# Performance work log

Measured on AMD Instinct MI355X. Metric: run time of the kernel, lower is better.

The kernel has to match this reference:

```python
import jax, jax.numpy as jnp
import numpy as np
import math

D = 512          # belief_dim
H = 128          # hidden_dim
R = 64           # relation_dim
M = 8192         # max_beliefs
N = 131072       # candidate pairs
INIT_BIAS = math.log(0.4 / 0.6) * -1.0  # = log(1.5) ~ 0.405465


def _linear_params(key, fan_in, fan_out):
    kw, kb = jax.random.split(key)
    bound = 1.0 / math.sqrt(fan_in)
    W = jax.random.uniform(kw, (fan_in, fan_out), minval=-bound, maxval=bound, dtype=jnp.float32)
    b = jax.random.uniform(kb, (fan_out,), minval=-bound, maxval=bound, dtype=jnp.float32)
    return W, b


def setup_inputs() -> dict:
    key = jax.random.key(0)
    ks = jax.random.split(key, 11)
    beliefs = jax.random.normal(ks[0], (M, D), dtype=jnp.float32)
    src_idx = jax.random.randint(ks[1], (N,), 0, M)
    tgt_idx = jax.random.randint(ks[2], (N,), 0, M)
    # proposal_net: 3D -> H -> H//2 -> 1  (last bias = log(1.5))
    pw1, pb1 = _linear_params(ks[3], 3 * D, H)
    pw2, pb2 = _linear_params(ks[4], H, H // 2)
    pw3, _ = _linear_params(ks[5], H // 2, 1)
    pb3 = jnp.full((1,), INIT_BIAS, dtype=jnp.float32)
    # direction_net: 3D -> H//2 -> 1 (sigmoid)
    dw1, db1 = _linear_params(ks[6], 3 * D, H // 2)
    dw2, db2 = _linear_params(ks[7], H // 2, 1)
    # relation_net: 3D -> H -> R
    rw1, rb1 = _linear_params(ks[8], 3 * D, H)
    rw2, rb2 = _linear_params(ks[9], H, R)
    return {
        "beliefs": beliefs, "src_idx": src_idx, "tgt_idx": tgt_idx,
        "pw1": pw1, "pb1": pb1, "pw2": pw2, "pb2": pb2, "pw3": pw3, "pb3": pb3,
        "dw1": dw1, "db1": db1, "dw2": dw2, "db2": db2,
        "rw1": rw1, "rb1": rb1, "rw2": rw2, "rb2": rb2,
    }


def reference(beliefs, src_idx, tgt_idx,
              pw1, pb1, pw2, pb2, pw3, pb3,
              dw1, db1, dw2, db2,
              rw1, rb1, rw2, rb2):
    src = beliefs[src_idx]                       # [N, D] gather
    tgt = beliefs[tgt_idx]                       # [N, D] gather
    feats = jnp.concatenate([src, tgt, jnp.abs(src - tgt)], axis=-1)  # [N, 3D]

    # proposal head -> edge probability
    h = jax.nn.relu(feats @ pw1 + pb1)
    h = jax.nn.relu(h @ pw2 + pb2)
    probs = jax.nn.sigmoid((h @ pw3 + pb3)[:, 0])                     # [N]

    # direction head -> angle in [0, pi/2]
    d = jax.nn.relu(feats @ dw1 + db1)
    directions = jax.nn.sigmoid((d @ dw2 + db2)[:, 0]) * (jnp.pi / 2)  # [N]

    # relation head -> initial relation vectors
    r = jax.nn.relu(feats @ rw1 + rb1)
    relations = r @ rw2 + rb2                                          # [N, R]

    return probs, directions, relations
```

## Files before the change

kernel.cpp:

```cpp
#include <hip/hip_runtime.h>
#include <hip/hip_bf16.h>


#define DD 512
#define K3 1536
#define ROWS 128
#define LDACT 328
#define LDH 72
#define BUFS 12288

typedef short bf16x8 __attribute__((ext_vector_type(8)));
typedef float f32x4 __attribute__((ext_vector_type(4)));

__device__ inline float b2f(short s) {
    union { float f; unsigned u; } v;
    v.u = ((unsigned)(unsigned short)s) << 16;
    return v.f;
}
__device__ inline short f2b(float f) {
    union { float fl; unsigned u; } v;
    v.fl = f;
    unsigned x = v.u;
    unsigned r = x + 0x7fffu + ((x >> 16) & 1u);
    return (short)(r >> 16);
}
__device__ inline short babsdiff(short a, short b) {
    union { float f; unsigned u; } v;
    v.f = b2f(a) - b2f(b);
    return (short)((v.u & 0x7fffffffu) >> 16);
}

__device__ __forceinline__ int sidx32(int seg, int rt, int lane) {
    return ((seg * 8 + rt) * 64 + lane) * 8;
}

__device__ __forceinline__ void writeStage(short* buf, int rtw, int lnw, int kcb,
                                           bf16x8 s0, bf16x8 s1,
                                           bf16x8 t0, bf16x8 t1) {
    bf16x8 a0, a1;
#pragma unroll
    for (int j = 0; j < 8; j++) {
        a0[j] = babsdiff(s0[j], t0[j]);
        a1[j] = babsdiff(s1[j], t1[j]);
    }
    int l0 = kcb * 16 + lnw, l1 = l0 + 16;
    *(bf16x8*)&buf[sidx32(0, rtw, l0)] = s0;
    *(bf16x8*)&buf[sidx32(0, rtw, l1)] = s1;
    *(bf16x8*)&buf[sidx32(1, rtw, l0)] = t0;
    *(bf16x8*)&buf[sidx32(1, rtw, l1)] = t1;
    *(bf16x8*)&buf[sidx32(2, rtw, l0)] = a0;
    *(bf16x8*)&buf[sidx32(2, rtw, l1)] = a1;
}

__device__ __forceinline__ void stage_f32(const float* bs, const float* bt,
                                          short* buf, int rtw, int lnw, int kcb) {
#pragma unroll
    for (int c = 0; c < 2; c++) {
        bf16x8 sb, tb, ab;
#pragma unroll
        for (int h = 0; h < 2; h++) {
            float4 s4 = ((const float4*)bs)[c * 2 + h];
            float4 t4 = ((const float4*)bt)[c * 2 + h];
            float ss[4] = {s4.x, s4.y, s4.z, s4.w};
            float tt[4] = {t4.x, t4.y, t4.z, t4.w};
#pragma unroll
            for (int e = 0; e < 4; e++) {
                int j = h * 4 + e;
                sb[j] = f2b(ss[e]);
                tb[j] = f2b(tt[e]);
                ab[j] = f2b(fabsf(ss[e] - tt[e]));
            }
        }
        int l16 = (kcb + c) * 16 + lnw;
        *(bf16x8*)&buf[sidx32(0, rtw, l16)] = sb;
        *(bf16x8*)&buf[sidx32(1, rtw, l16)] = tb;
        *(bf16x8*)&buf[sidx32(2, rtw, l16)] = ab;
    }
}

#define WT_ELEMS (320 * 1536)
#define P2T_OFF WT_ELEMS
#define R2T_OFF (WT_ELEMS + 64 * 128)
#define PREP_TOT (WT_ELEMS + 2 * 64 * 128)
#define BEL_ELEMS (8192 * 512)
#define BEL_OFF PREP_TOT

__global__ void prep_kernel(const float* __restrict__ pw1,
                            const float* __restrict__ dw1,
                            const float* __restrict__ rw1,
                            const float* __restrict__ pw2,
                            const float* __restrict__ rw2,
                            const float* __restrict__ beliefs,
                            short* __restrict__ ws, int total8) {
    int i8 = blockIdx.x * 256 + threadIdx.x;
    if (i8 >= total8) return;
    int i = i8 * 8;
    bf16x8 o;
    if (i < WT_ELEMS) {
        int n = i / K3, k = i - n * K3;
        const float* src;
        int stride, off;
        if (n < 128)      { src = pw1; stride = 128; off = n; }
        else if (n < 192) { src = dw1; stride = 64;  off = n - 128; }
        else              { src = rw1; stride = 128; off = n - 192; }
#pragma unroll
        for (int j = 0; j < 8; j++) o[j] = f2b(src[(k + j) * stride + off]);
    } else if (i < R2T_OFF) {
        int jj = i - P2T_OFF;
        int n = jj >> 7, k = jj & 127;
#pragma unroll
        for (int j = 0; j < 8; j++) o[j] = f2b(pw2[(k + j) * 64 + n]);
    } else if (i < PREP_TOT) {
        int jj = i - R2T_OFF;
        int n = jj >> 7, k = jj & 127;
#pragma unroll
        for (int j = 0; j < 8; j++) o[j] = f2b(rw2[(k + j) * 64 + n]);
    } else {
        const float4* b4 = (const float4*)(beliefs + (i - BEL_OFF));
        float4 x = b4[0], y = b4[1];
        float v[8] = {x.x, x.y, x.z, x.w, y.x, y.y, y.z, y.w};
#pragma unroll
        for (int j = 0; j < 8; j++) o[j] = f2b(v[j]);
    }
    *(bf16x8*)&ws[i] = o;
}

template<bool BF>
__global__ __launch_bounds__(256, 2) void edge_main(
    const float* __restrict__ beliefs, const short* __restrict__ bel16,
    const int* __restrict__ src_idx, const int* __restrict__ tgt_idx,
    const float* __restrict__ pb1, const float* __restrict__ db1,
    const float* __restrict__ rb1,
    const float* __restrict__ pb2, const float* __restrict__ pw3,
    const float* __restrict__ pb3,
    const float* __restrict__ dw2, const float* __restrict__ db2,
    const float* __restrict__ rb2,
    const short* __restrict__ WT, const short* __restrict__ pw2T,
    const short* __restrict__ rw2T,
    float* __restrict__ out, int N)
{
    __shared__ __align__(16) char smem_u[49152];
    __shared__ __align__(16) short h2s[64][LDH];
    __shared__ int sIdx[ROWS], tIdx[ROWS];

    short* As2 = (short*)smem_u;
    short (*acts)[LDACT] = (short (*)[LDACT])smem_u;

    const int t = threadIdx.x;
    const int r0 = blockIdx.x * ROWS;
    const int w = t >> 6, lane = t & 63, q = lane >> 4, ln = lane & 15;

    if (t < ROWS) sIdx[t] = src_idx[r0 + t] * DD;
    else tIdx[t - ROWS] = tgt_idx[r0 + t - ROWS] * DD;
    __syncthreads();

    f32x4 acc[5][8];
#pragma unroll
    for (int ct = 0; ct < 5; ct++)
#pragma unroll
        for (int rt = 0; rt < 8; rt++) acc[ct][rt] = (f32x4)(0.f);

    const int rrow = t >> 1, kh = t & 1;
    const int rtw = rrow >> 4, lnw = rrow & 15;
    const int kcb = kh * 2;
    const int srow = sIdx[rrow], trow = tIdx[rrow];

    if constexpr (BF) {
        const bf16x8* pS = (const bf16x8*)(bel16 + srow + kh * 16);
        const bf16x8* pT = (const bf16x8*)(bel16 + trow + kh * 16);
        writeStage(As2, rtw, lnw, kcb, pS[0], pS[1], pT[0], pT[1]);
    } else {
        stage_f32(beliefs + srow + kh * 16, beliefs + trow + kh * 16,
                  As2, rtw, lnw, kcb);
    }
    __syncthreads();

    for (int step = 0; step < 16; ++step) {
        short* bufC = As2 + (step & 1) * BUFS;
        short* bufN = As2 + ((step & 1) ^ 1) * BUFS;
        const int k0 = step * 32;
        const bool pf = (step < 15);
        bf16x8 ns0, ns1, nt0, nt1;

#pragma unroll
        for (int seg = 0; seg < 3; seg++) {
            bf16x8 bfr[5];
#pragma unroll
            for (int ct = 0; ct < 5; ct++) {
                int col = w * 80 + ct * 16 + ln;
                bfr[ct] = *(const bf16x8*)(WT + (size_t)col * K3 +
                                           seg * DD + k0 + q * 8);
            }
            if (seg == 2) {
                __builtin_amdgcn_sched_barrier(0);
                if constexpr (BF) {
                    if (pf) {
                        const bf16x8* pS = (const bf16x8*)(bel16 + srow + k0 + 32 + kh * 16);
                        const bf16x8* pT = (const bf16x8*)(bel16 + trow + k0 + 32 + kh * 16);
                        ns0 = pS[0]; ns1 = pS[1]; nt0 = pT[0]; nt1 = pT[1];
                    }
                }
                __builtin_amdgcn_sched_barrier(0);
            }
#pragma unroll
            for (int rt = 0; rt < 8; rt++) {
                bf16x8 af = *(const bf16x8*)&bufC[sidx32(seg, rt, lane)];
#pragma unroll
                for (int ct = 0; ct < 5; ct++)
                    acc[ct][rt] = __builtin_amdgcn_mfma_f32_16x16x32_bf16(
                        af, bfr[ct], acc[ct][rt], 0, 0, 0);
            }
        }
        if constexpr (BF) {
            if (pf) writeStage(bufN, rtw, lnw, kcb, ns0, ns1, nt0, nt1);
        } else {
            if (pf) stage_f32(beliefs + srow + k0 + 32 + kh * 16,
                              beliefs + trow + k0 + 32 + kh * 16,
                              bufN, rtw, lnw, kcb);
        }
        __syncthreads();
    }

#pragma unroll
    for (int h = 0; h < 2; h++) {
#pragma unroll
        for (int ct = 0; ct < 5; ct++) {
            int col = w * 80 + ct * 16 + ln;
            float bias = (col < 128) ? pb1[col]
                       : (col < 192) ? db1[col - 128]
                                     : rb1[col - 192];
#pragma unroll
            for (int rt4 = 0; rt4 < 4; rt4++)
#pragma unroll
                for (int i = 0; i < 4; i++) {
                    int lrow = rt4 * 16 + q * 4 + i;
                    float v = acc[ct][h * 4 + rt4][i] + bias;
                    acts[lrow][col] = f2b(fmaxf(v, 0.f));
                }
        }
        __syncthreads();

        {
            f32x4 rc[4];
#pragma unroll
            for (int rt = 0; rt < 4; rt++) rc[rt] = (f32x4)(0.f);
#pragma unroll
            for (int ks = 0; ks < 4; ks++) {
                bf16x8 bfr = *(const bf16x8*)(rw2T + (w * 16 + ln) * 128 +
                                              ks * 32 + q * 8);
#pragma unroll
                for (int rt = 0; rt < 4; rt++) {
                    bf16x8 afr = *(const bf16x8*)&acts[rt * 16 + ln][192 + ks * 32 + q * 8];
                    rc[rt] = __builtin_amdgcn_mfma_f32_16x16x32_bf16(afr, bfr, rc[rt], 0, 0, 0);
                }
            }
            int col = w * 16 + ln;
            float bias = rb2[col];
            float* rel = out + 2 * (size_t)N;
#pragma unroll
            for (int rt = 0; rt < 4; rt++)
#pragma unroll
                for (int i = 0; i < 4; i++) {
                    int grow = r0 + h * 64 + rt * 16 + q * 4 + i;
                    rel[(size_t)grow * 64 + col] = rc[rt][i] + bias;
                }
        }

        {
            f32x4 pc[4];
#pragma unroll
            for (int rt = 0; rt < 4; rt++) pc[rt] = (f32x4)(0.f);
#pragma unroll
            for (int ks = 0; ks < 4; ks++) {
                bf16x8 bfr = *(const bf16x8*)(pw2T + (w * 16 + ln) * 128 +
                                              ks * 32 + q * 8);
#pragma unroll
                for (int rt = 0; rt < 4; rt++) {
                    bf16x8 afr = *(const bf16x8*)&acts[rt * 16 + ln][0 + ks * 32 + q * 8];
                    pc[rt] = __builtin_amdgcn_mfma_f32_16x16x32_bf16(afr, bfr, pc[rt], 0, 0, 0);
                }
            }
            int col = w * 16 + ln;
            float bias = pb2[col];
#pragma unroll
            for (int rt = 0; rt < 4; rt++)
#pragma unroll
                for (int i = 0; i < 4; i++) {
                    int lrow = rt * 16 + q * 4 + i;
                    h2s[lrow][col] = f2b(fmaxf(pc[rt][i] + bias, 0.f));
                }
        }
        __syncthreads();

        if (t < 64) {
            float s = pb3[0];
#pragma unroll 8
            for (int k = 0; k < 64; k++) s += b2f(h2s[t][k]) * pw3[k];
            float pr = 1.f / (1.f + __expf(-s));
            out[r0 + h * 64 + t] = pr;
        } else if (t < 128) {
            int lrow = t - 64;
            float s = db2[0];
#pragma unroll 8
            for (int k = 0; k < 64; k++) s += b2f(acts[lrow][128 + k]) * dw2[k];
            float dir = (1.f / (1.f + __expf(-s))) * 1.57079632679489662f;
            out[(size_t)N + r0 + h * 64 + lrow] = dir;
        }
        __syncthreads();
    }
}

extern "C" void kernel_launch(void* const* d_in, const int* in_sizes, int n_in,
                              void* d_out, int out_size, void* d_ws, size_t ws_size,
                              hipStream_t stream) {
    const float* beliefs = (const float*)d_in[0];
    const int* src = (const int*)d_in[1];
    const int* tgt = (const int*)d_in[2];
    const float* pw1 = (const float*)d_in[3];
    const float* pb1 = (const float*)d_in[4];
    const float* pw2 = (const float*)d_in[5];
    const float* pb2 = (const float*)d_in[6];
    const float* pw3 = (const float*)d_in[7];
    const float* pb3 = (const float*)d_in[8];
    const float* dw1 = (const float*)d_in[9];
    const float* db1 = (const float*)d_in[10];
    const float* dw2 = (const float*)d_in[11];
    const float* db2 = (const float*)d_in[12];
    const float* rw1 = (const float*)d_in[13];
    const float* rb1 = (const float*)d_in[14];
    const float* rw2 = (const float*)d_in[15];
    const float* rb2 = (const float*)d_in[16];

    short* ws = (short*)d_ws;
    short* WT    = ws;
    short* pw2T  = ws + P2T_OFF;
    short* rw2T  = ws + R2T_OFF;
    short* bel16 = ws + BEL_OFF;
    const int N = in_sizes[1];

    const bool useBf = ws_size >= (size_t)(PREP_TOT + BEL_ELEMS) * sizeof(short);
    const int prepElems = useBf ? (PREP_TOT + BEL_ELEMS) : PREP_TOT;
    const int prep8 = prepElems / 8;

    prep_kernel<<<(prep8 + 255) / 256, 256, 0, stream>>>(
        pw1, dw1, rw1, pw2, rw2, beliefs, ws, prep8);

    if (useBf)
        edge_main<true><<<N / ROWS, 256, 0, stream>>>(
            beliefs, bel16, src, tgt, pb1, db1, rb1, pb2, pw3, pb3,
            dw2, db2, rb2, WT, pw2T, rw2T, (float*)d_out, N);
    else
        edge_main<false><<<N / ROWS, 256, 0, stream>>>(
            beliefs, bel16, src, tgt, pb1, db1, rb1, pb2, pw3, pb3,
            dw2, db2, rb2, WT, pw2T, rw2T, (float*)d_out, N);
}
```

Baseline: 270.3 us.

## Fold auxiliary LDS into main buffer for 3 blocks/CU, prefetch weights, set MFMA priority

Removes the separate h2s and index LDS arrays by aliasing them into the main shared buffer. This brings LDS per block down to 48KB so launch bounds can request 3 blocks per CU. An extra barrier is added to keep the aliasing safe. The seg-0 weight fragments for the next k-step are prefetched a step ahead, and the MFMA loop is wrapped in s_setprio. The risk is register pressure: the 160-float accumulator and the extra prefetch registers must fit under the tighter occupancy target, or the code may spill.

```diff
diff --git a/kernel.cpp b/kernel.cpp
--- a/kernel.cpp
+++ b/kernel.cpp
@@ -6,7 +6,6 @@
 #define K3 1536
 #define ROWS 128
 #define LDACT 328
-#define LDH 72
 #define BUFS 12288
 
 typedef short bf16x8 __attribute__((ext_vector_type(8)));
@@ -126,7 +125,7 @@
 }
 
 template<bool BF>
-__global__ __launch_bounds__(256, 2) void edge_main(
+__global__ __launch_bounds__(256, 3) void edge_main(
     const float* __restrict__ beliefs, const short* __restrict__ bel16,
     const int* __restrict__ src_idx, const int* __restrict__ tgt_idx,
     const float* __restrict__ pb1, const float* __restrict__ db1,
@@ -140,11 +139,11 @@
     float* __restrict__ out, int N)
 {
     __shared__ __align__(16) char smem_u[49152];
-    __shared__ __align__(16) short h2s[64][LDH];
-    __shared__ int sIdx[ROWS], tIdx[ROWS];
 
     short* As2 = (short*)smem_u;
     short (*acts)[LDACT] = (short (*)[LDACT])smem_u;
+    int* sIdx = (int*)smem_u;
+    int* tIdx = sIdx + ROWS;
 
     const int t = threadIdx.x;
     const int r0 = blockIdx.x * ROWS;
@@ -153,18 +152,25 @@
     if (t < ROWS) sIdx[t] = src_idx[r0 + t] * DD;
     else tIdx[t - ROWS] = tgt_idx[r0 + t - ROWS] * DD;
     __syncthreads();
-
-    f32x4 acc[5][8];
-#pragma unroll
-    for (int ct = 0; ct < 5; ct++)
-#pragma unroll
-        for (int rt = 0; rt < 8; rt++) acc[ct][rt] = (f32x4)(0.f);
 
     const int rrow = t >> 1, kh = t & 1;
     const int rtw = rrow >> 4, lnw = rrow & 15;
     const int kcb = kh * 2;
     const int srow = sIdx[rrow], trow = tIdx[rrow];
-
+    __syncthreads();
+
+    f32x4 acc[5][8];
+#pragma unroll
+    for (int ct = 0; ct < 5; ct++)
+#pragma unroll
+        for (int rt = 0; rt < 8; rt++) acc[ct][rt] = (f32x4)(0.f);
+
+    bf16x8 bfr0[5];
+#pragma unroll
+    for (int ct = 0; ct < 5; ct++) {
+        int col = w * 80 + ct * 16 + ln;
+        bfr0[ct] = *(const bf16x8*)(WT + (size_t)col * K3 + q * 8);
+    }
     if constexpr (BF) {
         const bf16x8* pS = (const bf16x8*)(bel16 + srow + kh * 16);
         const bf16x8* pT = (const bf16x8*)(bel16 + trow + kh * 16);
@@ -185,23 +191,35 @@
 #pragma unroll
         for (int seg = 0; seg < 3; seg++) {
             bf16x8 bfr[5];
-#pragma unroll
-            for (int ct = 0; ct < 5; ct++) {
-                int col = w * 80 + ct * 16 + ln;
-                bfr[ct] = *(const bf16x8*)(WT + (size_t)col * K3 +
-                                           seg * DD + k0 + q * 8);
+            if (seg == 0) {
+#pragma unroll
+                for (int ct = 0; ct < 5; ct++) bfr[ct] = bfr0[ct];
+            } else {
+#pragma unroll
+                for (int ct = 0; ct < 5; ct++) {
+                    int col = w * 80 + ct * 16 + ln;
+                    bfr[ct] = *(const bf16x8*)(WT + (size_t)col * K3 +
+                                               seg * DD + k0 + q * 8);
+                }
             }
             if (seg == 2) {
                 __builtin_amdgcn_sched_barrier(0);
-                if constexpr (BF) {
-                    if (pf) {
+                if (pf) {
+                    if constexpr (BF) {
                         const bf16x8* pS = (const bf16x8*)(bel16 + srow + k0 + 32 + kh * 16);
                         const bf16x8* pT = (const bf16x8*)(bel16 + trow + k0 + 32 + kh * 16);
                         ns0 = pS[0]; ns1 = pS[1]; nt0 = pT[0]; nt1 = pT[1];
                     }
+#pragma unroll
+                    for (int ct = 0; ct < 5; ct++) {
+                        int col = w * 80 + ct * 16 + ln;
+                        bfr0[ct] = *(const bf16x8*)(WT + (size_t)col * K3 +
+                                                    k0 + 32 + q * 8);
+                    }
                 }
                 __builtin_amdgcn_sched_barrier(0);
             }
+            __builtin_amdgcn_s_setprio(1);
 #pragma unroll
             for (int rt = 0; rt < 8; rt++) {
                 bf16x8 af = *(const bf16x8*)&bufC[sidx32(seg, rt, lane)];
@@ -210,6 +228,7 @@
                     acc[ct][rt] = __builtin_amdgcn_mfma_f32_16x16x32_bf16(
                         af, bfr[ct], acc[ct][rt], 0, 0, 0);
             }
+            __builtin_amdgcn_s_setprio(0);
         }
         if constexpr (BF) {
             if (pf) writeStage(bufN, rtw, lnw, kcb, ns0, ns1, nt0, nt1);
@@ -266,8 +285,8 @@
                 }
         }
 
+        f32x4 pc[4];
         {
-            f32x4 pc[4];
 #pragma unroll
             for (int rt = 0; rt < 4; rt++) pc[rt] = (f32x4)(0.f);
 #pragma unroll
@@ -280,6 +299,10 @@
                     pc[rt] = __builtin_amdgcn_mfma_f32_16x16x32_bf16(afr, bfr, pc[rt], 0, 0, 0);
                 }
             }
+        }
+        __syncthreads();
+
+        {
             int col = w * 16 + ln;
             float bias = pb2[col];
 #pragma unroll
@@ -287,7 +310,7 @@
 #pragma unroll
                 for (int i = 0; i < 4; i++) {
                     int lrow = rt * 16 + q * 4 + i;
-                    h2s[lrow][col] = f2b(fmaxf(pc[rt][i] + bias, 0.f));
+                    acts[lrow][col] = f2b(fmaxf(pc[rt][i] + bias, 0.f));
                 }
         }
         __syncthreads();
@@ -295,7 +318,7 @@
         if (t < 64) {
             float s = pb3[0];
 #pragma unroll 8
-            for (int k = 0; k < 64; k++) s += b2f(h2s[t][k]) * pw3[k];
+            for (int k = 0; k < 64; k++) s += b2f(acts[t][k]) * pw3[k];
             float pr = 1.f / (1.f + __expf(-s));
             out[r0 + h * 64 + t] = pr;
         } else if (t < 128) {
```

Result: slower. 963.5 us (+256.5%).

## Halve rows per block to 64 and raise occupancy to three blocks per CU

Applied to the files above, without the earlier changes.

Each block now handles 64 candidate rows instead of 128. This halves the accumulator registers and the staging buffers, and the h2s and index arrays are folded into the shared activation buffer so LDS use drops to about 41KB. The launch bounds are raised to 3 blocks per CU to hide gather latency, and s_setprio is added around the MFMA loops. The cost is that each block reuses the weight tiles loaded from global/L2 over half as many rows, doubling total weight traffic.

```diff
diff --git a/kernel.cpp b/kernel.cpp
--- a/kernel.cpp
+++ b/kernel.cpp
@@ -4,10 +4,9 @@
 
 #define DD 512
 #define K3 1536
-#define ROWS 128
+#define RB 64
 #define LDACT 328
-#define LDH 72
-#define BUFS 12288
+#define BUFS 6144
 
 typedef short bf16x8 __attribute__((ext_vector_type(8)));
 typedef float f32x4 __attribute__((ext_vector_type(4)));
@@ -30,52 +29,36 @@
     return (short)((v.u & 0x7fffffffu) >> 16);
 }
 
-__device__ __forceinline__ int sidx32(int seg, int rt, int lane) {
-    return ((seg * 8 + rt) * 64 + lane) * 8;
-}
-
-__device__ __forceinline__ void writeStage(short* buf, int rtw, int lnw, int kcb,
-                                           bf16x8 s0, bf16x8 s1,
-                                           bf16x8 t0, bf16x8 t1) {
-    bf16x8 a0, a1;
-#pragma unroll
-    for (int j = 0; j < 8; j++) {
-        a0[j] = babsdiff(s0[j], t0[j]);
-        a1[j] = babsdiff(s1[j], t1[j]);
-    }
-    int l0 = kcb * 16 + lnw, l1 = l0 + 16;
-    *(bf16x8*)&buf[sidx32(0, rtw, l0)] = s0;
-    *(bf16x8*)&buf[sidx32(0, rtw, l1)] = s1;
-    *(bf16x8*)&buf[sidx32(1, rtw, l0)] = t0;
-    *(bf16x8*)&buf[sidx32(1, rtw, l1)] = t1;
-    *(bf16x8*)&buf[sidx32(2, rtw, l0)] = a0;
-    *(bf16x8*)&buf[sidx32(2, rtw, l1)] = a1;
+__device__ __forceinline__ int sidx4(int seg, int rt, int lane) {
+    return ((seg * 4 + rt) * 64 + lane) * 8;
+}
+
+__device__ __forceinline__ void writeStage(short* buf, int rtw, int lpos,
+                                           bf16x8 s8, bf16x8 t8) {
+    bf16x8 a8;
+#pragma unroll
+    for (int j = 0; j < 8; j++) a8[j] = babsdiff(s8[j], t8[j]);
+    *(bf16x8*)&buf[sidx4(0, rtw, lpos)] = s8;
+    *(bf16x8*)&buf[sidx4(1, rtw, lpos)] = t8;
+    *(bf16x8*)&buf[sidx4(2, rtw, lpos)] = a8;
 }
 
 __device__ __forceinline__ void stage_f32(const float* bs, const float* bt,
-                                          short* buf, int rtw, int lnw, int kcb) {
-#pragma unroll
-    for (int c = 0; c < 2; c++) {
-        bf16x8 sb, tb, ab;
-#pragma unroll
-        for (int h = 0; h < 2; h++) {
-            float4 s4 = ((const float4*)bs)[c * 2 + h];
-            float4 t4 = ((const float4*)bt)[c * 2 + h];
-            float ss[4] = {s4.x, s4.y, s4.z, s4.w};
-            float tt[4] = {t4.x, t4.y, t4.z, t4.w};
-#pragma unroll
-            for (int e = 0; e < 4; e++) {
-                int j = h * 4 + e;
-                sb[j] = f2b(ss[e]);
-                tb[j] = f2b(tt[e]);
-                ab[j] = f2b(fabsf(ss[e] - tt[e]));
-            }
-        }
-        int l16 = (kcb + c) * 16 + lnw;
-        *(bf16x8*)&buf[sidx32(0, rtw, l16)] = sb;
-        *(bf16x8*)&buf[sidx32(1, rtw, l16)] = tb;
-        *(bf16x8*)&buf[sidx32(2, rtw, l16)] = ab;
-    }
+                                          short* buf, int rtw, int lpos) {
+    bf16x8 s8, t8;
+#pragma unroll
+    for (int h = 0; h < 2; h++) {
+        float4 s4 = ((const float4*)bs)[h];
+        float4 t4 = ((const float4*)bt)[h];
+        float ss[4] = {s4.x, s4.y, s4.z, s4.w};
+        float tt[4] = {t4.x, t4.y, t4.z, t4.w};
+#pragma unroll
+        for (int e = 0; e < 4; e++) {
+            s8[h * 4 + e] = f2b(ss[e]);
+            t8[h * 4 + e] = f2b(tt[e]);
+        }
+    }
+    writeStage(buf, rtw, lpos, s8, t8);
 }
 
 #define WT_ELEMS (320 * 1536)
@@ -126,7 +109,7 @@
 }
 
 template<bool BF>
-__global__ __launch_bounds__(256, 2) void edge_main(
+__global__ __launch_bounds__(256, 3) void edge_main(
     const float* __restrict__ beliefs, const short* __restrict__ bel16,
     const int* __restrict__ src_idx, const int* __restrict__ tgt_idx,
     const float* __restrict__ pb1, const float* __restrict__ db1,
@@ -139,39 +122,40 @@
     const short* __restrict__ rw2T,
     float* __restrict__ out, int N)
 {
-    __shared__ __align__(16) char smem_u[49152];
-    __shared__ __align__(16) short h2s[64][LDH];
-    __shared__ int sIdx[ROWS], tIdx[ROWS];
+    __shared__ __align__(16) char smem_u[41984];
 
     short* As2 = (short*)smem_u;
     short (*acts)[LDACT] = (short (*)[LDACT])smem_u;
+    int* sIdx = (int*)smem_u;
+    int* tIdx = sIdx + RB;
 
     const int t = threadIdx.x;
-    const int r0 = blockIdx.x * ROWS;
+    const int r0 = blockIdx.x * RB;
     const int w = t >> 6, lane = t & 63, q = lane >> 4, ln = lane & 15;
 
-    if (t < ROWS) sIdx[t] = src_idx[r0 + t] * DD;
-    else tIdx[t - ROWS] = tgt_idx[r0 + t - ROWS] * DD;
-    __syncthreads();
-
-    f32x4 acc[5][8];
+    if (t < RB) sIdx[t] = src_idx[r0 + t] * DD;
+    else if (t < 2 * RB) tIdx[t - RB] = tgt_idx[r0 + t - RB] * DD;
+    __syncthreads();
+
+    const int rr = t >> 2, cc = t & 3;
+    const int rtw = rr >> 4;
+    const int lpos = cc * 16 + (rr & 15);
+    const int srow = sIdx[rr], trow = tIdx[rr];
+    __syncthreads();
+
+    f32x4 acc[5][4];
 #pragma unroll
     for (int ct = 0; ct < 5; ct++)
 #pragma unroll
-        for (int rt = 0; rt < 8; rt++) acc[ct][rt] = (f32x4)(0.f);
-
-    const int rrow = t >> 1, kh = t & 1;
-    const int rtw = rrow >> 4, lnw = rrow & 15;
-    const int kcb = kh * 2;
-    const int srow = sIdx[rrow], trow = tIdx[rrow];
+        for (int rt = 0; rt < 4; rt++) acc[ct][rt] = (f32x4)(0.f);
 
     if constexpr (BF) {
-        const bf16x8* pS = (const bf16x8*)(bel16 + srow + kh * 16);
-        const bf16x8* pT = (const bf16x8*)(bel16 + trow + kh * 16);
-        writeStage(As2, rtw, lnw, kcb, pS[0], pS[1], pT[0], pT[1]);
+        bf16x8 s8 = *(const bf16x8*)(bel16 + srow + cc * 8);
+        bf16x8 t8 = *(const bf16x8*)(bel16 + trow + cc * 8);
+        writeStage(As2, rtw, lpos, s8, t8);
     } else {
-        stage_f32(beliefs + srow + kh * 16, beliefs + trow + kh * 16,
-                  As2, rtw, lnw, kcb);
+        stage_f32(beliefs + srow + cc * 8, beliefs + trow + cc * 8,
+                  As2, rtw, lpos);
     }
     __syncthreads();
 
@@ -180,7 +164,7 @@
         short* bufN = As2 + ((step & 1) ^ 1) * BUFS;
         const int k0 = step * 32;
         const bool pf = (step < 15);
-        bf16x8 ns0, ns1, nt0, nt1;
+        bf16x8 ns8, nt8;
 
 #pragma unroll
         for (int seg = 0; seg < 3; seg++) {
@@ -193,120 +177,121 @@
             }
             if (seg == 2) {
                 __builtin_amdgcn_sched_barrier(0);
-                if constexpr (BF) {
-                    if (pf) {
-                        const bf16x8* pS = (const bf16x8*)(bel16 + srow + k0 + 32 + kh * 16);
-                        const bf16x8* pT = (const bf16x8*)(bel16 + trow + k0 + 32 + kh * 16);
-                        ns0 = pS[0]; ns1 = pS[1]; nt0 = pT[0]; nt1 = pT[1];
+                if (pf) {
+                    if constexpr (BF) {
+                        ns8 = *(const bf16x8*)(bel16 + srow + k0 + 32 + cc * 8);
+                        nt8 = *(const bf16x8*)(bel16 + trow + k0 + 32 + cc * 8);
                     }
                 }
                 __builtin_amdgcn_sched_barrier(0);
             }
-#pragma unroll
-            for (int rt = 0; rt < 8; rt++) {
-                bf16x8 af = *(const bf16x8*)&bufC[sidx32(seg, rt, lane)];
+            __builtin_amdgcn_s_setprio(1);
+#pragma unroll
+            for (int rt = 0; rt < 4; rt++) {
+                bf16x8 af = *(const bf16x8*)&bufC[sidx4(seg, rt, lane)];
 #pragma unroll
                 for (int ct = 0; ct < 5; ct++)
                     acc[ct][rt] = __builtin_amdgcn_mfma_f32_16x16x32_bf16(
                         af, bfr[ct], acc[ct][rt], 0, 0, 0);
             }
+            __builtin_amdgcn_s_setprio(0);
         }
         if constexpr (BF) {
-            if (pf) writeStage(bufN, rtw, lnw, kcb, ns0, ns1, nt0, nt1);
+            if (pf) writeStage(bufN, rtw, lpos, ns8, nt8);
         } else {
-            if (pf) stage_f32(beliefs + srow + k0 + 32 + kh * 16,
-                              beliefs + trow + k0 + 32 + kh * 16,
-                              bufN, rtw, lnw, kcb);
+            if (pf) stage_f32(beliefs + srow + k0 + 32 + cc * 8,
+                              beliefs + trow + k0 + 32 + cc * 8,
+                              bufN, rtw, lpos);
         }
         __syncthreads();
     }
 
 #pragma unroll
-    for (int h = 0; h < 2; h++) {
-#pragma unroll
-        for (int ct = 0; ct < 5; ct++) {
-            int col = w * 80 + ct * 16 + ln;
-            float bias = (col < 128) ? pb1[col]
-                       : (col < 192) ? db1[col - 128]
-                                     : rb1[col - 192];
-#pragma unroll
-            for (int rt4 = 0; rt4 < 4; rt4++)
-#pragma unroll
-                for (int i = 0; i < 4; i++) {
-                    int lrow = rt4 * 16 + q * 4 + i;
-                    float v = acc[ct][h * 4 + rt4][i] + bias;
-                    acts[lrow][col] = f2b(fmaxf(v, 0.f));
-                }
-        }
-        __syncthreads();
-
-        {
-            f32x4 rc[4];
-#pragma unroll
-            for (int rt = 0; rt < 4; rt++) rc[rt] = (f32x4)(0.f);
-#pragma unroll
-            for (int ks = 0; ks < 4; ks++) {
-                bf16x8 bfr = *(const bf16x8*)(rw2T + (w * 16 + ln) * 128 +
-                                              ks * 32 + q * 8);
-#pragma unroll
-                for (int rt = 0; rt < 4; rt++) {
-                    bf16x8 afr = *(const bf16x8*)&acts[rt * 16 + ln][192 + ks * 32 + q * 8];
-                    rc[rt] = __builtin_amdgcn_mfma_f32_16x16x32_bf16(afr, bfr, rc[rt], 0, 0, 0);
-                }
-            }
-            int col = w * 16 + ln;
-            float bias = rb2[col];
-            float* rel = out + 2 * (size_t)N;
-#pragma unroll
-            for (int rt = 0; rt < 4; rt++)
-#pragma unroll
-                for (int i = 0; i < 4; i++) {
-                    int grow = r0 + h * 64 + rt * 16 + q * 4 + i;
-                    rel[(size_t)grow * 64 + col] = rc[rt][i] + bias;
-                }
-        }
-
-        {
-            f32x4 pc[4];
-#pragma unroll
-            for (int rt = 0; rt < 4; rt++) pc[rt] = (f32x4)(0.f);
-#pragma unroll
-            for (int ks = 0; ks < 4; ks++) {
-                bf16x8 bfr = *(const bf16x8*)(pw2T + (w * 16 + ln) * 128 +
-                                              ks * 32 + q * 8);
-#pragma unroll
-                for (int rt = 0; rt < 4; rt++) {
-                    bf16x8 afr = *(const bf16x8*)&acts[rt * 16 + ln][0 + ks * 32 + q * 8];
-                    pc[rt] = __builtin_amdgcn_mfma_f32_16x16x32_bf16(afr, bfr, pc[rt], 0, 0, 0);
-                }
-            }
-            int col = w * 16 + ln;
-            float bias = pb2[col];
-#pragma unroll
-            for (int rt = 0; rt < 4; rt++)
-#pragma unroll
-                for (int i = 0; i < 4; i++) {
-                    int lrow = rt * 16 + q * 4 + i;
-                    h2s[lrow][col] = f2b(fmaxf(pc[rt][i] + bias, 0.f));
-                }
-        }
-        __syncthreads();
-
-        if (t < 64) {
-            float s = pb3[0];
+    for (int ct = 0; ct < 5; ct++) {
+        int col = w * 80 + ct * 16 + ln;
+        float bias = (col < 128) ? pb1[col]
+                   : (col < 192) ? db1[col - 128]
+                                 : rb1[col - 192];
+#pragma unroll
+        for (int rt = 0; rt < 4; rt++)
+#pragma unroll
+            for (int i = 0; i < 4; i++) {
+                int lrow = rt * 16 + q * 4 + i;
+                float v = acc[ct][rt][i] + bias;
+                acts[lrow][col] = f2b(fmaxf(v, 0.f));
+            }
+    }
+    __syncthreads();
+
+    {
+        f32x4 rc[4];
+#pragma unroll
+        for (int rt = 0; rt < 4; rt++) rc[rt] = (f32x4)(0.f);
+#pragma unroll
+        for (int ks = 0; ks < 4; ks++) {
+            bf16x8 bfr = *(const bf16x8*)(rw2T + (w * 16 + ln) * 128 +
+                                          ks * 32 + q * 8);
+#pragma unroll
+            for (int rt = 0; rt < 4; rt++) {
+                bf16x8 afr = *(const bf16x8*)&acts[rt * 16 + ln][192 + ks * 32 + q * 8];
+                rc[rt] = __builtin_amdgcn_mfma_f32_16x16x32_bf16(afr, bfr, rc[rt], 0, 0, 0);
+            }
+        }
+        int col = w * 16 + ln;
+        float bias = rb2[col];
+        float* rel = out + 2 * (size_t)N;
+#pragma unroll
+        for (int rt = 0; rt < 4; rt++)
+#pragma unroll
+            for (int i = 0; i < 4; i++) {
+                int grow = r0 + rt * 16 + q * 4 + i;
+                rel[(size_t)grow * 64 + col] = rc[rt][i] + bias;
+            }
+    }
+
+    f32x4 pc[4];
+    {
+#pragma unroll
+        for (int rt = 0; rt < 4; rt++) pc[rt] = (f32x4)(0.f);
+#pragma unroll
+        for (int ks = 0; ks < 4; ks++) {
+            bf16x8 bfr = *(const bf16x8*)(pw2T + (w * 16 + ln) * 128 +
+                                          ks * 32 + q * 8);
+#pragma unroll
+            for (int rt = 0; rt < 4; rt++) {
+                bf16x8 afr = *(const bf16x8*)&acts[rt * 16 + ln][0 + ks * 32 + q * 8];
+                pc[rt] = __builtin_amdgcn_mfma_f32_16x16x32_bf16(afr, bfr, pc[rt], 0, 0, 0);
+            }
+        }
+    }
+    __syncthreads();
+
+    {
+        int col = w * 16 + ln;
+        float bias = pb2[col];
+#pragma unroll
+        for (int rt = 0; rt < 4; rt++)
+#pragma unroll
+            for (int i = 0; i < 4; i++) {
+                int lrow = rt * 16 + q * 4 + i;
+                acts[lrow][col] = f2b(fmaxf(pc[rt][i] + bias, 0.f));
+            }
+    }
+    __syncthreads();
+
+    if (t < 64) {
+        float s = pb3[0];
 #pragma unroll 8
-            for (int k = 0; k < 64; k++) s += b2f(h2s[t][k]) * pw3[k];
-            float pr = 1.f / (1.f + __expf(-s));
-            out[r0 + h * 64 + t] = pr;
-        } else if (t < 128) {
-            int lrow = t - 64;
-            float s = db2[0];
+        for (int k = 0; k < 64; k++) s += b2f(acts[t][k]) * pw3[k];
+        float pr = 1.f / (1.f + __expf(-s));
+        out[r0 + t] = pr;
+    } else if (t < 128) {
+        int lrow = t - 64;
+        float s = db2[0];
 #pragma unroll 8
-            for (int k = 0; k < 64; k++) s += b2f(acts[lrow][128 + k]) * dw2[k];
-            float dir = (1.f / (1.f + __expf(-s))) * 1.57079632679489662f;
-            out[(size_t)N + r0 + h * 64 + lrow] = dir;
-        }
-        __syncthreads();
+        for (int k = 0; k < 64; k++) s += b2f(acts[lrow][128 + k]) * dw2[k];
+        float dir = (1.f / (1.f + __expf(-s))) * 1.57079632679489662f;
+        out[(size_t)N + r0 + lrow] = dir;
     }
 }
 
@@ -346,11 +331,11 @@
         pw1, dw1, rw1, pw2, rw2, beliefs, ws, prep8);
 
     if (useBf)
-        edge_main<true><<<N / ROWS, 256, 0, stream>>>(
+        edge_main<true><<<N / RB, 256, 0, stream>>>(
             beliefs, bel16, src, tgt, pb1, db1, rb1, pb2, pw3, pb3,
             dw2, db2, rb2, WT, pw2T, rw2T, (float*)d_out, N);
     else
-        edge_main<false><<<N / ROWS, 256, 0, stream>>>(
+        edge_main<false><<<N / RB, 256, 0, stream>>>(
             beliefs, bel16, src, tgt, pb1, db1, rb1, pb2, pw3, pb3,
             dw2, db2, rb2, WT, pw2T, rw2T, (float*)d_out, N);
 }
```

After: 344.9 us. 27.6% more time.
